# Kernel optimization log

Measured on AMD Instinct MI355X. Metric: run time of the kernel, lower is better.

Reference implementation:

```python
import jax, jax.numpy as jnp
import numpy as np

D_MODEL = 1024
NHEAD = 16
EPS = 1e-5


def pos_embed(x, pos):
    # Faithful, vectorized form of the sparse rotation matrix in the source.
    # Source builds rot[..., i, i+1] = sin(pos*i*omega) for even i and
    # rot[..., i, i-1] = cos(pos*i*omega) for odd i, then contracts the feature
    # dim of x against the rotation (intended einsum 'btf,btfd->btd').
    # Resulting column j: even j <- x[..., j+1]*cos(pos*(j+1)*omega),
    #                     odd  j <- x[..., j-1]*sin(pos*(j-1)*omega).
    d = x.shape[-1]
    omega = jnp.pi / d
    i_even = jnp.arange(0, d, 2, dtype=x.dtype)   # even rows -> odd output cols (sin)
    i_odd = jnp.arange(1, d, 2, dtype=x.dtype)    # odd rows  -> even output cols (cos)
    p = pos[..., None]  # (L,B,1)
    sin_part = jnp.sin(p * i_even * omega) * x[..., 0::2]  # -> odd columns
    cos_part = jnp.cos(p * i_odd * omega) * x[..., 1::2]   # -> even columns
    # interleave: even col = cos_part, odd col = sin_part
    return jnp.stack([cos_part, sin_part], axis=-1).reshape(x.shape)


def layer_norm_eps(x, w, b):
    # Source uses torch.var default (unbiased, ddof=1)
    mean = jnp.mean(x, axis=-1, keepdims=True)
    var = jnp.var(x, axis=-1, keepdims=True, ddof=1)
    return w * (x - mean) / jnp.sqrt(var + EPS) + b


def mha(q, k, v, w_qkv, b_qkv, w_o, b_o, nhead):
    L, B, E = q.shape
    S = k.shape[0]
    hd = E // nhead
    wq, wk, wv = jnp.split(w_qkv, 3, axis=0)
    bq, bk, bv = jnp.split(b_qkv, 3, axis=0)
    qp = (q @ wq.T + bq).reshape(L, B, nhead, hd).transpose(1, 2, 0, 3)  # (B,h,L,hd)
    kp = (k @ wk.T + bk).reshape(S, B, nhead, hd).transpose(1, 2, 0, 3)
    vp = (v @ wv.T + bv).reshape(S, B, nhead, hd).transpose(1, 2, 0, 3)
    scale = jnp.asarray(1.0 / np.sqrt(hd), q.dtype)
    scores = jnp.einsum('bhld,bhsd->bhls', qp, kp) * scale
    attn = jax.nn.softmax(scores, axis=-1)
    out = jnp.einsum('bhls,bhsd->bhld', attn, vp)
    out = out.transpose(2, 0, 1, 3).reshape(L, B, E) @ w_o.T + b_o
    ws = attn.mean(axis=1)  # average over heads, torch default
    return out, ws


def setup_inputs() -> dict:
    key = jax.random.key(0)
    ks = jax.random.split(key, 16)
    T, S, B, E, FF = 1024, 1024, 4, D_MODEL, 4096
    sd = 0.02
    return {
        'tgt': jax.random.normal(ks[0], (T, B, E), jnp.float32),
        'memory': jax.random.normal(ks[1], (S, B, E), jnp.float32),
        'pos': jax.random.uniform(ks[2], (S, B), jnp.float32) * S,
        'query_pos': jax.random.uniform(ks[3], (T, B), jnp.float32) * T,
        'w_qkv_self': jax.random.normal(ks[4], (3 * E, E), jnp.float32) * sd,
        'b_qkv_self': jnp.zeros((3 * E,), jnp.float32),
        'w_o_self': jax.random.normal(ks[5], (E, E), jnp.float32) * sd,
        'b_o_self': jnp.zeros((E,), jnp.float32),
        'w_qkv_cross': jax.random.normal(ks[6], (3 * E, E), jnp.float32) * sd,
        'b_qkv_cross': jnp.zeros((3 * E,), jnp.float32),
        'w_o_cross': jax.random.normal(ks[7], (E, E), jnp.float32) * sd,
        'b_o_cross': jnp.zeros((E,), jnp.float32),
        'w1': jax.random.normal(ks[8], (FF, E), jnp.float32) * sd,
        'b1': jnp.zeros((FF,), jnp.float32),
        'w2': jax.random.normal(ks[9], (E, FF), jnp.float32) * sd,
        'b2': jnp.zeros((E,), jnp.float32),
        'g1': jnp.ones((E,), jnp.float32),
        'beta1': jnp.zeros((E,), jnp.float32),
        'g2': jnp.ones((E,), jnp.float32),
        'beta2': jnp.zeros((E,), jnp.float32),
    }


def reference(tgt, memory, pos, query_pos,
              w_qkv_self, b_qkv_self, w_o_self, b_o_self,
              w_qkv_cross, b_qkv_cross, w_o_cross, b_o_cross,
              w1, b1, w2, b2, g1, beta1, g2, beta2):
    # normalize_before=False, residual=True, dropout inactive (eval)
    qk = pos_embed(tgt, query_pos)
    tgt2, _ = mha(qk, qk, tgt, w_qkv_self, b_qkv_self, w_o_self, b_o_self, NHEAD)
    tgt = tgt + tgt2
    tgt = layer_norm_eps(tgt, g1, beta1)
    tgt2, ws = mha(pos_embed(tgt, query_pos), pos_embed(memory, pos), memory,
                   w_qkv_cross, b_qkv_cross, w_o_cross, b_o_cross, NHEAD)
    tgt = tgt + tgt2
    tgt = layer_norm_eps(tgt, g2, beta2)
    tgt2 = jax.nn.relu(tgt @ w1.T + b1) @ w2.T + b2
    tgt = tgt + tgt2
    return tgt, ws
```

## Files before the change

### kernel.cpp

```cpp
#include <hip/hip_runtime.h>

typedef unsigned short u16;
typedef __attribute__((ext_vector_type(8))) short short8;
typedef __attribute__((ext_vector_type(8))) unsigned short u16x8;
typedef __attribute__((ext_vector_type(4))) float f32x4;

#define GLOAD16(SRC, DST) __builtin_amdgcn_global_load_lds( \
    (const __attribute__((address_space(1))) void*)(SRC),   \
    (__attribute__((address_space(3))) void*)(DST), 16, 0, 0)

#define SWZ(BKv, r) ((BKv) == 32 ? (((r) >> 1) & 3) : ((r) & 7))

#define QSCALE 0.18033688011112042f

__device__ __forceinline__ u16 f2bf(float f) {
  union { float f; unsigned u; } v; v.f = f;
  unsigned r = v.u + 0x7fffu + ((v.u >> 16) & 1u);
  return (u16)(r >> 16);
}
__device__ __forceinline__ float bf2f(u16 h) {
  union { unsigned u; float f; } v; v.u = ((unsigned)h) << 16;
  return v.f;
}

__global__ __launch_bounds__(256) void wcvt_kernel(const float* __restrict__ s0,
                                                   const float* __restrict__ s1,
                                                   const float* __restrict__ s2,
                                                   const float* __restrict__ s3,
                                                   const float* __restrict__ s4,
                                                   const float* __restrict__ s5,
                                                   u16* __restrict__ dst) {
  long i = ((long)blockIdx.x * 256 + threadIdx.x) * 4;
  const float* src; long off;
  if (i < 3145728)        { src = s0; off = 0; }
  else if (i < 4194304)   { src = s1; off = 3145728; }
  else if (i < 7340032)   { src = s2; off = 4194304; }
  else if (i < 8388608)   { src = s3; off = 7340032; }
  else if (i < 12582912)  { src = s4; off = 8388608; }
  else                    { src = s5; off = 12582912; }
  float4 v = *(const float4*)(src + (i - off));
  ushort4 o; o.x = f2bf(v.x); o.y = f2bf(v.y); o.z = f2bf(v.z); o.w = f2bf(v.w);
  *(ushort4*)(dst + i) = o;
}

__global__ __launch_bounds__(256) void pos_embed_kernel(const float* __restrict__ x,
                                                        const float* __restrict__ pos,
                                                        u16* __restrict__ out,
                                                        u16* __restrict__ out2,
                                                        u16* __restrict__ raw) {
  int m = blockIdx.x;
  int tid = threadIdx.x;
  float p = pos[m];
  long base = ((long)m << 10);
  int j = tid * 4;
  float4 xv = *(const float4*)(x + base + j);
  const float inv = 1.0f / 2048.0f;
  float r0 = p * (float)(j + 0) * inv;
  float r1 = p * (float)(j + 1) * inv;
  float r2 = p * (float)(j + 2) * inv;
  float r3 = p * (float)(j + 3) * inv;
  float s1 = __builtin_amdgcn_sinf(r0 - floorf(r0));
  float c0 = __builtin_amdgcn_cosf(r1 - floorf(r1));
  float s3 = __builtin_amdgcn_sinf(r2 - floorf(r2));
  float c2 = __builtin_amdgcn_cosf(r3 - floorf(r3));
  ushort4 o;
  o.x = f2bf(c0 * xv.y);
  o.y = f2bf(s1 * xv.x);
  o.z = f2bf(c2 * xv.w);
  o.w = f2bf(s3 * xv.z);
  *(ushort4*)(out + base + j) = o;
  if (out2) *(ushort4*)(out2 + base + j) = o;
  if (raw) {
    ushort4 rw; rw.x = f2bf(xv.x); rw.y = f2bf(xv.y); rw.z = f2bf(xv.z); rw.w = f2bf(xv.w);
    *(ushort4*)(raw + base + j) = rw;
  }
}

__global__ __launch_bounds__(256) void split_qkv_kernel(const u16* __restrict__ P,
                                                        u16* __restrict__ Qb,
                                                        u16* __restrict__ Kb,
                                                        u16* __restrict__ Vtb) {
  long e = ((long)blockIdx.x * 256 + threadIdx.x) * 8;
  int m = (int)(e / 3072);
  int n = (int)(e % 3072);
  int t = m >> 2, b = m & 3;
  int sec = n >> 10, nn = n & 1023;
  int h = nn >> 6, d = nn & 63;
  long bh = b * 16 + h;
  u16x8 v = *(const u16x8*)(P + e);
  if (sec == 0) {
    *(u16x8*)(Qb + (bh << 16) + ((long)t << 6) + d) = v;
  } else if (sec == 1) {
    *(u16x8*)(Kb + (bh << 16) + ((long)t << 6) + d) = v;
  } else {
    u16* dst = Vtb + (bh << 16) + ((long)d << 10) + t;
#pragma unroll
    for (int q = 0; q < 8; q++) dst[(long)q << 10] = v[q];
  }
}

__global__ __launch_bounds__(256) void fattn_kernel(const u16* __restrict__ Q,
                                                    const u16* __restrict__ K,
                                                    const u16* __restrict__ Vt,
                                                    u16* __restrict__ AO,
                                                    float2* __restrict__ Ml) {
  __shared__ u16 lK[2][4096];
  __shared__ u16 lV[2][4096];
  __shared__ u16 lP[4][1024];
  const int tid = threadIdx.x, lane = tid & 63, wid = tid >> 6;
  const int nb = gridDim.x * gridDim.y;
  const int orig = blockIdx.y * gridDim.x + blockIdx.x;
  const int swz = (orig & 7) * (nb >> 3) + (orig >> 3);
  const int qt = swz & 15;
  const int bh = swz >> 4;
  const int b = bh >> 4, h = bh & 15;
  const u16* Qp = Q + ((long)bh << 16);
  const u16* Kp = K + ((long)bh << 16);
  const u16* Vp = Vt + ((long)bh << 16);
  const int q0 = qt << 6;
  const int cr = lane >> 4;

  short8 af0, af1;
  {
    const u16* qs = Qp + (long)(q0 + wid * 16 + (lane & 15)) * 64 + cr * 8;
    af0 = *(const short8*)qs;
    af1 = *(const short8*)(qs + 32);
  }

  float m[4] = {-1e30f, -1e30f, -1e30f, -1e30f};
  float l[4] = {0.f, 0.f, 0.f, 0.f};
  f32x4 acco[4] = {};

  auto stage = [&](int bufi, int kv) {
    int s0 = kv << 6;
#pragma unroll
    for (int it = 0; it < 2; it++) {
      int c = it * 256 + tid;
      int row = c >> 3, ch = c & 7;
      int sch = (ch ^ (row & 7)) * 8;
      GLOAD16(Kp + (long)(s0 + row) * 64 + sch, &lK[bufi][c * 8]);
      GLOAD16(Vp + (long)row * 1024 + s0 + sch, &lV[bufi][c * 8]);
    }
  };

  stage(0, 0);
  __syncthreads();
  int buf = 0;
  for (int kv = 0; kv < 16; kv++) {
    if (kv < 15) stage(buf ^ 1, kv + 1);
    f32x4 accs[4];
    __builtin_amdgcn_s_setprio(1);
#pragma unroll
    for (int j = 0; j < 4; j++) {
      int sr = j * 16 + (lane & 15);
      const short8 kf0 = *(const short8*)&lK[buf][sr * 64 + ((cr ^ (sr & 7)) * 8)];
      const short8 kf1 = *(const short8*)&lK[buf][sr * 64 + (((4 + cr) ^ (sr & 7)) * 8)];
      f32x4 zz = {};
      zz = __builtin_amdgcn_mfma_f32_16x16x32_bf16(af0, kf0, zz, 0, 0, 0);
      accs[j] = __builtin_amdgcn_mfma_f32_16x16x32_bf16(af1, kf1, zz, 0, 0, 0);
    }
    __builtin_amdgcn_s_setprio(0);
    float tm[4];
#pragma unroll
    for (int r = 0; r < 4; r++)
      tm[r] = fmaxf(fmaxf(accs[0][r], accs[1][r]), fmaxf(accs[2][r], accs[3][r]));
#pragma unroll
    for (int o = 1; o < 16; o <<= 1)
#pragma unroll
      for (int r = 0; r < 4; r++) tm[r] = fmaxf(tm[r], __shfl_xor(tm[r], o));
    float growth = fmaxf(fmaxf(tm[0] - m[0], tm[1] - m[1]),
                         fmaxf(tm[2] - m[2], tm[3] - m[3]));
    if (!__all(growth <= 8.0f)) {
#pragma unroll
      for (int r = 0; r < 4; r++) {
        float mn = fmaxf(m[r], tm[r]);
        float f = __builtin_amdgcn_exp2f(m[r] - mn);
        m[r] = mn; l[r] *= f;
        acco[0][r] *= f; acco[1][r] *= f; acco[2][r] *= f; acco[3][r] *= f;
      }
    }
    float rs[4] = {0.f, 0.f, 0.f, 0.f};
#pragma unroll
    for (int j = 0; j < 4; j++)
#pragma unroll
      for (int r = 0; r < 4; r++) {
        float p = __builtin_amdgcn_exp2f(accs[j][r] - m[r]);
        accs[j][r] = p;
        rs[r] += p;
      }
#pragma unroll
    for (int o = 1; o < 16; o <<= 1)
#pragma unroll
      for (int r = 0; r < 4; r++) rs[r] += __shfl_xor(rs[r], o);
#pragma unroll
    for (int r = 0; r < 4; r++) l[r] += rs[r];
    u16* pw = lP[wid];
#pragma unroll
    for (int jp = 0; jp < 2; jp++)
#pragma unroll
      for (int r = 0; r < 4; r++) {
        int qr = (lane >> 4) * 4 + r;
        unsigned pk;
        asm("v_cvt_pk_bf16_f32 %0, %1, %2"
            : "=v"(pk) : "v"(accs[2 * jp][r]), "v"(accs[2 * jp + 1][r]));
        int sA = (2 * jp) * 16 + (lane & 15);
        int sB = sA + 16;
        pw[qr * 64 + (((sA >> 3) ^ (qr & 7)) * 8) + (sA & 7)] = (u16)pk;
        pw[qr * 64 + (((sB >> 3) ^ (qr & 7)) * 8) + (sB & 7)] = (u16)(pk >> 16);
      }
    {
      int ql = lane & 15;
      const u16* pr = &lP[wid][ql * 64];
      short8 pa0 = *(const short8*)&pr[(cr ^ (ql & 7)) * 8];
      short8 pa1 = *(const short8*)&pr[((4 + cr) ^ (ql & 7)) * 8];
      __builtin_amdgcn_s_setprio(1);
#pragma unroll
      for (int j = 0; j < 4; j++) {
        int dr = j * 16 + (lane & 15);
        const short8 vf0 = *(const short8*)&lV[buf][dr * 64 + ((cr ^ (dr & 7)) * 8)];
        const short8 vf1 = *(const short8*)&lV[buf][dr * 64 + (((4 + cr) ^ (dr & 7)) * 8)];
        acco[j] = __builtin_amdgcn_mfma_f32_16x16x32_bf16(pa0, vf0, acco[j], 0, 0, 0);
        acco[j] = __builtin_amdgcn_mfma_f32_16x16x32_bf16(pa1, vf1, acco[j], 0, 0, 0);
      }
      __builtin_amdgcn_s_setprio(0);
    }
    __syncthreads();
    buf ^= 1;
  }
  float invl[4];
#pragma unroll
  for (int r = 0; r < 4; r++) invl[r] = 1.0f / l[r];
#pragma unroll
  for (int j = 0; j < 4; j++)
#pragma unroll
    for (int r = 0; r < 4; r++) {
      int t = q0 + wid * 16 + (lane >> 4) * 4 + r;
      int e = (b << 10) + (h << 6) + j * 16 + (lane & 15);
      AO[(long)t * 4096 + e] = f2bf(acco[j][r] * invl[r]);
    }
  if (Ml && (lane & 15) == 0) {
#pragma unroll
    for (int r = 0; r < 4; r++) {
      int t = q0 + wid * 16 + (lane >> 4) * 4 + r;
      Ml[((long)bh << 10) + t] = make_float2(m[r], invl[r]);
    }
  }
}

__global__ __launch_bounds__(256) void wsrec_kernel(const u16* __restrict__ Q,
                                                    const u16* __restrict__ K,
                                                    const float2* __restrict__ Ml,
                                                    float* __restrict__ ws) {
  __shared__ u16 lK[2][4096];
  const int tid = threadIdx.x, lane = tid & 63, wid = tid >> 6;
  const int nb = gridDim.x * gridDim.y;
  const int orig = blockIdx.y * gridDim.x + blockIdx.x;
  const int swz = (orig & 7) * (nb >> 3) + (orig >> 3);
  const int st = swz & 15, lt = swz >> 4;
  const int b = blockIdx.z;
  const int s0 = st << 6, l0 = lt << 6;
  const int cr = lane >> 4;

  auto stage = [&](int bufi, int h) {
    const u16* Kp = K + (((long)(b * 16 + h)) << 16);
#pragma unroll
    for (int it = 0; it < 2; it++) {
      int c = it * 256 + tid;
      int row = c >> 3, ch = c & 7;
      GLOAD16(Kp + (long)(s0 + row) * 64 + ((ch ^ (row & 7)) * 8), &lK[bufi][c * 8]);
    }
  };

  f32x4 wacc[4] = {};
  stage(0, 0);
  __syncthreads();
  int buf = 0;
  for (int h = 0; h < 16; h++) {
    if (h < 15) stage(buf ^ 1, h + 1);
    const int bh = b * 16 + h;
    short8 af0, af1;
    {
      const u16* qs = Q + ((long)bh << 16) + (long)(l0 + wid * 16 + (lane & 15)) * 64 + cr * 8;
      af0 = *(const short8*)qs;
      af1 = *(const short8*)(qs + 32);
    }
    f32x4 accs[4];
    __builtin_amdgcn_s_setprio(1);
#pragma unroll
    for (int j = 0; j < 4; j++) {
      int sr = j * 16 + (lane & 15);
      const short8 kf0 = *(const short8*)&lK[buf][sr * 64 + ((cr ^ (sr & 7)) * 8)];
      const short8 kf1 = *(const short8*)&lK[buf][sr * 64 + (((4 + cr) ^ (sr & 7)) * 8)];
      f32x4 zz = {};
      zz = __builtin_amdgcn_mfma_f32_16x16x32_bf16(af0, kf0, zz, 0, 0, 0);
      accs[j] = __builtin_amdgcn_mfma_f32_16x16x32_bf16(af1, kf1, zz, 0, 0, 0);
    }
    __builtin_amdgcn_s_setprio(0);
    float mm[4], il[4];
#pragma unroll
    for (int r = 0; r < 4; r++) {
      float2 v = Ml[((long)bh << 10) + l0 + wid * 16 + (lane >> 4) * 4 + r];
      mm[r] = v.x; il[r] = v.y * 0.0625f;
    }
#pragma unroll
    for (int j = 0; j < 4; j++)
#pragma unroll
      for (int r = 0; r < 4; r++)
        wacc[j][r] += __builtin_amdgcn_exp2f(accs[j][r] - mm[r]) * il[r];
    __syncthreads();
    buf ^= 1;
  }
#pragma unroll
  for (int j = 0; j < 4; j++)
#pragma unroll
    for (int r = 0; r < 4; r++) {
      int li = l0 + wid * 16 + (lane >> 4) * 4 + r;
      int si = s0 + j * 16 + (lane & 15);
      ws[((long)b << 20) + (long)li * 1024 + si] = wacc[j][r];
    }
}

__global__ __launch_bounds__(256) void ln_kernel(const float* __restrict__ X,
                                                 const float* __restrict__ D1,
                                                 const float* __restrict__ D2,
                                                 const float* __restrict__ bo,
                                                 const float* __restrict__ g,
                                                 const float* __restrict__ be,
                                                 float* __restrict__ out,
                                                 u16* __restrict__ bfout) {
  int mrow = blockIdx.x;
  int tid = threadIdx.x, lane = tid & 63, wid = tid >> 6;
  long base = ((long)mrow << 10);
  float4 a = *(const float4*)(X + base + tid * 4);
  float4 b = *(const float4*)(D1 + base + tid * 4);
  float x0 = a.x + b.x, x1 = a.y + b.y, x2 = a.z + b.z, x3 = a.w + b.w;
  if (D2) {
    float4 c = *(const float4*)(D2 + base + tid * 4);
    x0 += c.x; x1 += c.y; x2 += c.z; x3 += c.w;
  }
  if (bo) {
    float4 c = *(const float4*)(bo + tid * 4);
    x0 += c.x; x1 += c.y; x2 += c.z; x3 += c.w;
  }
  float s = x0 + x1 + x2 + x3;
#pragma unroll
  for (int o = 32; o; o >>= 1) s += __shfl_xor(s, o);
  __shared__ float red[4];
  if (lane == 0) red[wid] = s;
  __syncthreads();
  float mean = (red[0] + red[1] + red[2] + red[3]) * (1.0f / 1024.0f);
  float d0 = x0 - mean, d1 = x1 - mean, d2 = x2 - mean, d3 = x3 - mean;
  float ss = d0 * d0 + d1 * d1 + d2 * d2 + d3 * d3;
#pragma unroll
  for (int o = 32; o; o >>= 1) ss += __shfl_xor(ss, o);
  __syncthreads();
  if (lane == 0) red[wid] = ss;
  __syncthreads();
  float var = (red[0] + red[1] + red[2] + red[3]) * (1.0f / 1023.0f);
  float sc = 1.0f / sqrtf(var + 1e-5f);
  float4 gv = *(const float4*)(g + tid * 4);
  float4 bv = *(const float4*)(be + tid * 4);
  float y0 = gv.x * d0 * sc + bv.x;
  float y1 = gv.y * d1 * sc + bv.y;
  float y2 = gv.z * d2 * sc + bv.z;
  float y3 = gv.w * d3 * sc + bv.w;
  float4 o4; o4.x = y0; o4.y = y1; o4.z = y2; o4.w = y3;
  *(float4*)(out + base + tid * 4) = o4;
  if (bfout) {
    ushort4 hh; hh.x = f2bf(y0); hh.y = f2bf(y1); hh.z = f2bf(y2); hh.w = f2bf(y3);
    *(ushort4*)(bfout + base + tid * 4) = hh;
  }
}

__global__ __launch_bounds__(256) void add3_kernel(const float* __restrict__ X,
                                                   const float* __restrict__ P0,
                                                   const float* __restrict__ P1,
                                                   const float* __restrict__ b,
                                                   float* __restrict__ out) {
  long i = ((long)blockIdx.x * 256 + threadIdx.x) * 4;
  int col = (int)(i & 1023);
  float4 x = *(const float4*)(X + i);
  float4 p = *(const float4*)(P0 + i);
  float4 q = *(const float4*)(P1 + i);
  float4 bb = *(const float4*)(b + col);
  float4 o;
  o.x = x.x + p.x + q.x + bb.x;
  o.y = x.y + p.y + q.y + bb.y;
  o.z = x.z + p.z + q.z + bb.z;
  o.w = x.w + p.w + q.w + bb.w;
  *(float4*)(out + i) = o;
}

template <int BM, int BN, int BK, int WR, int WC, int NT, int DB>
__global__ __launch_bounds__(NT)
void gemm_bt_kernel(const u16* __restrict__ A, const u16* __restrict__ B,
                    void* __restrict__ C, const float* __restrict__ bias,
                    int lda, int ldb, int ldc, int K,
                    long sAz, long sBz, long sCz, long sbz,
                    float alpha, int flags) {
  constexpr int WTM = BM / WR, WTN = BN / WC;
  constexpr int FM = WTM / 16, FN = WTN / 16;
  constexpr int NC = BK / 8;
  __shared__ u16 lA[DB][BM * BK];
  __shared__ u16 lB[DB][BN * BK];
  const int tid = threadIdx.x, lane = tid & 63, wid = tid >> 6;
  const int wr = wid / WC, wc = wid % WC;
  const int z = blockIdx.z;

  const int nwg = gridDim.x * gridDim.y;
  const int orig = blockIdx.y * gridDim.x + blockIdx.x;
  const int qq = nwg >> 3, rr = nwg & 7;
  const int xcd = orig & 7, idx = orig >> 3;
  const int swz = (xcd < rr ? xcd * (qq + 1) : rr * (qq + 1) + (xcd - rr) * qq) + idx;
  const int bxs = swz % gridDim.x;
  const int bys = swz / gridDim.x;

  const u16* Ab = A + z * sAz + (long)bys * BM * lda;
  const u16* Bb = B + z * sBz + (long)bxs * BN * ldb;

  f32x4 acc[FM][FN] = {};

  auto stage = [&](int bufi, int k0) {
#pragma unroll
    for (int c0 = 0; c0 < BM * NC; c0 += NT) {
      int c = c0 + tid;
      if ((BM * NC) % NT == 0 || c < BM * NC) {
        int row = c / NC, ch = c % NC;
        int sch = ch ^ SWZ(BK, row);
        GLOAD16(Ab + (long)row * lda + k0 + sch * 8, &lA[bufi][c * 8]);
      }
    }
#pragma unroll
    for (int c0 = 0; c0 < BN * NC; c0 += NT) {
      int c = c0 + tid;
      if ((BN * NC) % NT == 0 || c < BN * NC) {
        int row = c / NC, ch = c % NC;
        int sch = ch ^ SWZ(BK, row);
        GLOAD16(Bb + (long)row * ldb + k0 + sch * 8, &lB[bufi][c * 8]);
      }
    }
  };

  auto compute = [&](int bufi) {
#pragma unroll
    for (int kk = 0; kk < BK / 32; kk++) {
      short8 afv[FM], bfv[FN];
#pragma unroll
      for (int i = 0; i < FM; i++) {
        int row = wr * WTM + i * 16 + (lane & 15);
        int ch = kk * 4 + (lane >> 4);
        afv[i] = *(const short8*)&lA[bufi][row * BK + ((ch ^ SWZ(BK, row)) * 8)];
      }
#pragma unroll
      for (int j = 0; j < FN; j++) {
        int row = wc * WTN + j * 16 + (lane & 15);
        int ch = kk * 4 + (lane >> 4);
        bfv[j] = *(const short8*)&lB[bufi][row * BK + ((ch ^ SWZ(BK, row)) * 8)];
      }
#pragma unroll
      for (int i = 0; i < FM; i++)
#pragma unroll
        for (int j = 0; j < FN; j++)
          acc[i][j] = __builtin_amdgcn_mfma_f32_16x16x32_bf16(afv[i], bfv[j], acc[i][j], 0, 0, 0);
    }
  };

  const int nk = K / BK;
  if (DB == 2) {
    stage(0, 0);
    __syncthreads();
    int cur = 0;
    for (int t = 0; t < nk; t++) {
      if (t + 1 < nk) stage(cur ^ 1, (t + 1) * BK);
      compute(cur);
      __syncthreads();
      cur ^= 1;
    }
  } else {
    for (int t = 0; t < nk; t++) {
      stage(0, t * BK);
      __syncthreads();
      compute(0);
      __syncthreads();
    }
  }

  const long rbase = (long)bys * BM + wr * WTM;
  const int cbase = bxs * BN + wc * WTN;
  const float* bz = bias ? (bias + z * sbz) : nullptr;
#pragma unroll
  for (int i = 0; i < FM; i++)
#pragma unroll
    for (int j = 0; j < FN; j++)
#pragma unroll
      for (int r = 0; r < 4; r++) {
        long row = rbase + i * 16 + ((lane >> 4) * 4 + r);
        int col = cbase + j * 16 + (lane & 15);
        float v = acc[i][j][r];
        if (!(flags & 8)) v *= alpha;
        if (flags & 1) v += bz[col];
        if ((flags & 8) && z == 0) v *= alpha;
        if (flags & 2) v = fmaxf(v, 0.0f);
        long off = (long)z * sCz + row * (long)ldc + col;
        if (flags & 4) ((float*)C)[off] = v;
        else ((u16*)C)[off] = f2bf(v);
      }
}

extern "C" void kernel_launch(void* const* d_in, const int* in_sizes, int n_in,
                              void* d_out, int out_size, void* d_ws, size_t ws_size,
                              hipStream_t stream) {
  const float* tgt  = (const float*)d_in[0];
  const float* mem  = (const float*)d_in[1];
  const float* pos  = (const float*)d_in[2];
  const float* qpos = (const float*)d_in[3];
  const float* wqkvS = (const float*)d_in[4];
  const float* bqkvS = (const float*)d_in[5];
  const float* woS   = (const float*)d_in[6];
  const float* boS   = (const float*)d_in[7];
  const float* wqkvC = (const float*)d_in[8];
  const float* bqkvC = (const float*)d_in[9];
  const float* woC   = (const float*)d_in[10];
  const float* boC   = (const float*)d_in[11];
  const float* w1  = (const float*)d_in[12];
  const float* b1  = (const float*)d_in[13];
  const float* w2  = (const float*)d_in[14];
  const float* b2  = (const float*)d_in[15];
  const float* g1  = (const float*)d_in[16];
  const float* be1 = (const float*)d_in[17];
  const float* g2  = (const float*)d_in[18];
  const float* be2 = (const float*)d_in[19];

  const size_t MB = 1024ull * 1024ull;
  float* out0 = (float*)d_out;
  float* wsout = out0 + 4194304;

  char* W = (char*)d_ws;
  u16* wb = (u16*)W;
  u16* wqkvS_b = wb;
  u16* woS_b   = wb + 3145728;
  u16* wqkvC_b = wb + 4194304;
  u16* woC_b   = wb + 7340032;
  u16* w1_b    = wb + 8388608;
  u16* w2_b    = wb + 12582912;
  float* Xf   = (float*)(W + 32 * MB);
  float* OPar = (float*)(W + 48 * MB);
  u16* Pq  = (u16*)(W + 48 * MB);
  u16* bf1 = (u16*)(W + 80 * MB);
  u16* bf2 = (u16*)(W + 88 * MB);
  u16* bf3 = (u16*)(W + 96 * MB);
  float2* Ml = (float2*)(W + 96 * MB);
  u16* Qb  = (u16*)(W + 104 * MB);
  u16* Kb  = (u16*)(W + 112 * MB);
  u16* Vtb = (u16*)(W + 120 * MB);
  u16* AOb = (u16*)(W + 128 * MB);
  u16* F1  = (u16*)(W + 104 * MB);

  wcvt_kernel<<<16384, 256, 0, stream>>>(wqkvS, woS, wqkvC, woC, w1, w2, wb);

  pos_embed_kernel<<<4096, 256, 0, stream>>>(tgt, qpos, bf1, bf2, bf3);
  gemm_bt_kernel<128, 128, 32, 2, 4, 512, 2><<<dim3(8, 32, 3), 512, 0, stream>>>(
      bf1, wqkvS_b, Pq, bqkvS, 1024, 1024, 3072, 1024,
      4194304, 1048576, 1024, 1024, QSCALE, 1 | 8);
  split_qkv_kernel<<<6144, 256, 0, stream>>>(Pq, Qb, Kb, Vtb);
  fattn_kernel<<<dim3(16, 64), 256, 0, stream>>>(Qb, Kb, Vtb, AOb, nullptr);
  gemm_bt_kernel<128, 128, 32, 2, 4, 512, 2><<<dim3(8, 32, 2), 512, 0, stream>>>(
      AOb, woS_b, OPar, nullptr, 1024, 1024, 1024, 512,
      512, 512, 4194304, 0, 1.0f, 4);
  ln_kernel<<<4096, 256, 0, stream>>>(tgt, OPar, OPar + 4194304, boS, g1, be1, Xf, nullptr);

  pos_embed_kernel<<<4096, 256, 0, stream>>>(Xf, qpos, bf1, nullptr, nullptr);
  pos_embed_kernel<<<4096, 256, 0, stream>>>(mem, pos, bf2, nullptr, bf3);
  gemm_bt_kernel<128, 128, 32, 2, 4, 512, 2><<<dim3(8, 32, 3), 512, 0, stream>>>(
      bf1, wqkvC_b, Pq, bqkvC, 1024, 1024, 3072, 1024,
      4194304, 1048576, 1024, 1024, QSCALE, 1 | 8);
  split_qkv_kernel<<<6144, 256, 0, stream>>>(Pq, Qb, Kb, Vtb);
  fattn_kernel<<<dim3(16, 64), 256, 0, stream>>>(Qb, Kb, Vtb, AOb, Ml);
  wsrec_kernel<<<dim3(16, 16, 4), 256, 0, stream>>>(Qb, Kb, Ml, wsout);
  gemm_bt_kernel<128, 128, 32, 2, 4, 512, 2><<<dim3(8, 32, 2), 512, 0, stream>>>(
      AOb, woC_b, OPar, nullptr, 1024, 1024, 1024, 512,
      512, 512, 4194304, 0, 1.0f, 4);
  ln_kernel<<<4096, 256, 0, stream>>>(Xf, OPar, OPar + 4194304, boC, g2, be2, Xf, bf1);

  gemm_bt_kernel<128, 128, 32, 2, 4, 512, 2><<<dim3(32, 32, 1), 512, 0, stream>>>(
      bf1, w1_b, F1, b1, 1024, 1024, 4096, 1024, 0, 0, 0, 0, 1.0f, 1 | 2);
  gemm_bt_kernel<128, 128, 32, 2, 4, 512, 2><<<dim3(8, 32, 2), 512, 0, stream>>>(
      F1, w2_b, OPar, nullptr, 4096, 4096, 1024, 2048,
      2048, 2048, 4194304, 0, 1.0f, 4);
  add3_kernel<<<4096, 256, 0, stream>>>(Xf, OPar, OPar + 4194304, b2, out0);
}
```

Measured before the change: 473.8 us.

## Transpose QK^T MFMA operands in flash attention and raise GEMM K-tile

The flash-attention kernel swaps the A and B operands of the score MFMA, so each lane now holds one query row's scores across four keys. The row max and row sum then need only two cross-lane shuffles instead of a 16-lane butterfly over four rows, and P is written to LDS as packed 64-bit stores instead of scattered 16-bit stores. Per-row rescale factors and the final 1/l are broadcast with __shfl to match the transposed output layout. Separately, four of the GEMM launches (QKV projections, FFN1, FFN2) move from a K-tile of 32 to 64, which halves the K-loop iterations but uses more LDS per block and may lower occupancy.

```diff
diff --git a/kernel.cpp b/kernel.cpp
--- a/kernel.cpp
+++ b/kernel.cpp
@@ -127,8 +127,7 @@
     af1 = *(const short8*)(qs + 32);
   }
 
-  float m[4] = {-1e30f, -1e30f, -1e30f, -1e30f};
-  float l[4] = {0.f, 0.f, 0.f, 0.f};
+  float m = -1e30f, l = 0.f;
   f32x4 acco[4] = {};
 
   auto stage = [&](int bufi, int kv) {
@@ -156,58 +155,56 @@
       const short8 kf0 = *(const short8*)&lK[buf][sr * 64 + ((cr ^ (sr & 7)) * 8)];
       const short8 kf1 = *(const short8*)&lK[buf][sr * 64 + (((4 + cr) ^ (sr & 7)) * 8)];
       f32x4 zz = {};
-      zz = __builtin_amdgcn_mfma_f32_16x16x32_bf16(af0, kf0, zz, 0, 0, 0);
-      accs[j] = __builtin_amdgcn_mfma_f32_16x16x32_bf16(af1, kf1, zz, 0, 0, 0);
+      zz = __builtin_amdgcn_mfma_f32_16x16x32_bf16(kf0, af0, zz, 0, 0, 0);
+      accs[j] = __builtin_amdgcn_mfma_f32_16x16x32_bf16(kf1, af1, zz, 0, 0, 0);
     }
     __builtin_amdgcn_s_setprio(0);
-    float tm[4];
-#pragma unroll
-    for (int r = 0; r < 4; r++)
-      tm[r] = fmaxf(fmaxf(accs[0][r], accs[1][r]), fmaxf(accs[2][r], accs[3][r]));
-#pragma unroll
-    for (int o = 1; o < 16; o <<= 1)
-#pragma unroll
-      for (int r = 0; r < 4; r++) tm[r] = fmaxf(tm[r], __shfl_xor(tm[r], o));
-    float growth = fmaxf(fmaxf(tm[0] - m[0], tm[1] - m[1]),
-                         fmaxf(tm[2] - m[2], tm[3] - m[3]));
-    if (!__all(growth <= 8.0f)) {
+    float tm = fmaxf(fmaxf(fmaxf(accs[0][0], accs[0][1]), fmaxf(accs[0][2], accs[0][3])),
+                     fmaxf(fmaxf(accs[1][0], accs[1][1]), fmaxf(accs[1][2], accs[1][3])));
+    float tm2 = fmaxf(fmaxf(fmaxf(accs[2][0], accs[2][1]), fmaxf(accs[2][2], accs[2][3])),
+                      fmaxf(fmaxf(accs[3][0], accs[3][1]), fmaxf(accs[3][2], accs[3][3])));
+    tm = fmaxf(tm, tm2);
+    tm = fmaxf(tm, __shfl_xor(tm, 16));
+    tm = fmaxf(tm, __shfl_xor(tm, 32));
+    if (!__all(tm - m <= 8.0f)) {
+      float mn = fmaxf(m, tm);
+      float f = __builtin_amdgcn_exp2f(m - mn);
+      m = mn; l *= f;
 #pragma unroll
       for (int r = 0; r < 4; r++) {
-        float mn = fmaxf(m[r], tm[r]);
-        float f = __builtin_amdgcn_exp2f(m[r] - mn);
-        m[r] = mn; l[r] *= f;
-        acco[0][r] *= f; acco[1][r] *= f; acco[2][r] *= f; acco[3][r] *= f;
-      }
-    }
-    float rs[4] = {0.f, 0.f, 0.f, 0.f};
+        float fr = __shfl(f, cr * 4 + r);
+        acco[0][r] *= fr; acco[1][r] *= fr; acco[2][r] *= fr; acco[3][r] *= fr;
+      }
+    }
+    float rs = 0.f;
 #pragma unroll
     for (int j = 0; j < 4; j++)
 #pragma unroll
       for (int r = 0; r < 4; r++) {
-        float p = __builtin_amdgcn_exp2f(accs[j][r] - m[r]);
+        float p = __builtin_amdgcn_exp2f(accs[j][r] - m);
         accs[j][r] = p;
-        rs[r] += p;
-      }
-#pragma unroll
-    for (int o = 1; o < 16; o <<= 1)
-#pragma unroll
-      for (int r = 0; r < 4; r++) rs[r] += __shfl_xor(rs[r], o);
-#pragma unroll
-    for (int r = 0; r < 4; r++) l[r] += rs[r];
-    u16* pw = lP[wid];
-#pragma unroll
-    for (int jp = 0; jp < 2; jp++)
-#pragma unroll
-      for (int r = 0; r < 4; r++) {
-        int qr = (lane >> 4) * 4 + r;
-        unsigned pk;
+        rs += p;
+      }
+    rs += __shfl_xor(rs, 16);
+    rs += __shfl_xor(rs, 32);
+    l += rs;
+    {
+      u16* pw = lP[wid];
+      int q = lane & 15;
+      int rowoff = q * 64;
+      int qs7 = q & 7;
+#pragma unroll
+      for (int j = 0; j < 4; j++) {
+        uint2 pk;
         asm("v_cvt_pk_bf16_f32 %0, %1, %2"
-            : "=v"(pk) : "v"(accs[2 * jp][r]), "v"(accs[2 * jp + 1][r]));
-        int sA = (2 * jp) * 16 + (lane & 15);
-        int sB = sA + 16;
-        pw[qr * 64 + (((sA >> 3) ^ (qr & 7)) * 8) + (sA & 7)] = (u16)pk;
-        pw[qr * 64 + (((sB >> 3) ^ (qr & 7)) * 8) + (sB & 7)] = (u16)(pk >> 16);
-      }
+            : "=v"(pk.x) : "v"(accs[j][0]), "v"(accs[j][1]));
+        asm("v_cvt_pk_bf16_f32 %0, %1, %2"
+            : "=v"(pk.y) : "v"(accs[j][2]), "v"(accs[j][3]));
+        int chunk = 2 * j + (cr >> 1);
+        int idx = rowoff + ((chunk ^ qs7) * 8) + 4 * (cr & 1);
+        *(uint2*)(pw + idx) = pk;
+      }
+    }
     {
       int ql = lane & 15;
       const u16* pr = &lP[wid][ql * 64];
@@ -227,23 +224,21 @@
     __syncthreads();
     buf ^= 1;
   }
-  float invl[4];
-#pragma unroll
-  for (int r = 0; r < 4; r++) invl[r] = 1.0f / l[r];
+  float invl = 1.0f / l;
+  float ilr[4];
+#pragma unroll
+  for (int r = 0; r < 4; r++) ilr[r] = __shfl(invl, cr * 4 + r);
 #pragma unroll
   for (int j = 0; j < 4; j++)
 #pragma unroll
     for (int r = 0; r < 4; r++) {
-      int t = q0 + wid * 16 + (lane >> 4) * 4 + r;
+      int t = q0 + wid * 16 + cr * 4 + r;
       int e = (b << 10) + (h << 6) + j * 16 + (lane & 15);
-      AO[(long)t * 4096 + e] = f2bf(acco[j][r] * invl[r]);
-    }
-  if (Ml && (lane & 15) == 0) {
-#pragma unroll
-    for (int r = 0; r < 4; r++) {
-      int t = q0 + wid * 16 + (lane >> 4) * 4 + r;
-      Ml[((long)bh << 10) + t] = make_float2(m[r], invl[r]);
-    }
+      AO[(long)t * 4096 + e] = f2bf(acco[j][r] * ilr[r]);
+    }
+  if (Ml && lane < 16) {
+    int t = q0 + wid * 16 + lane;
+    Ml[((long)bh << 10) + t] = make_float2(m, invl);
   }
 }
 
@@ -559,7 +554,7 @@
   wcvt_kernel<<<16384, 256, 0, stream>>>(wqkvS, woS, wqkvC, woC, w1, w2, wb);
 
   pos_embed_kernel<<<4096, 256, 0, stream>>>(tgt, qpos, bf1, bf2, bf3);
-  gemm_bt_kernel<128, 128, 32, 2, 4, 512, 2><<<dim3(8, 32, 3), 512, 0, stream>>>(
+  gemm_bt_kernel<128, 128, 64, 2, 4, 512, 2><<<dim3(8, 32, 3), 512, 0, stream>>>(
       bf1, wqkvS_b, Pq, bqkvS, 1024, 1024, 3072, 1024,
       4194304, 1048576, 1024, 1024, QSCALE, 1 | 8);
   split_qkv_kernel<<<6144, 256, 0, stream>>>(Pq, Qb, Kb, Vtb);
@@ -571,7 +566,7 @@
 
   pos_embed_kernel<<<4096, 256, 0, stream>>>(Xf, qpos, bf1, nullptr, nullptr);
   pos_embed_kernel<<<4096, 256, 0, stream>>>(mem, pos, bf2, nullptr, bf3);
-  gemm_bt_kernel<128, 128, 32, 2, 4, 512, 2><<<dim3(8, 32, 3), 512, 0, stream>>>(
+  gemm_bt_kernel<128, 128, 64, 2, 4, 512, 2><<<dim3(8, 32, 3), 512, 0, stream>>>(
       bf1, wqkvC_b, Pq, bqkvC, 1024, 1024, 3072, 1024,
       4194304, 1048576, 1024, 1024, QSCALE, 1 | 8);
   split_qkv_kernel<<<6144, 256, 0, stream>>>(Pq, Qb, Kb, Vtb);
@@ -582,9 +577,9 @@
       512, 512, 4194304, 0, 1.0f, 4);
   ln_kernel<<<4096, 256, 0, stream>>>(Xf, OPar, OPar + 4194304, boC, g2, be2, Xf, bf1);
 
-  gemm_bt_kernel<128, 128, 32, 2, 4, 512, 2><<<dim3(32, 32, 1), 512, 0, stream>>>(
+  gemm_bt_kernel<128, 128, 64, 2, 4, 512, 2><<<dim3(32, 32, 1), 512, 0, stream>>>(
       bf1, w1_b, F1, b1, 1024, 1024, 4096, 1024, 0, 0, 0, 0, 1.0f, 1 | 2);
-  gemm_bt_kernel<128, 128, 32, 2, 4, 512, 2><<<dim3(8, 32, 2), 512, 0, stream>>>(
+  gemm_bt_kernel<128, 128, 64, 2, 4, 512, 2><<<dim3(8, 32, 2), 512, 0, stream>>>(
       F1, w2_b, OPar, nullptr, 4096, 4096, 1024, 2048,
       2048, 2048, 4194304, 0, 1.0f, 4);
   add3_kernel<<<4096, 256, 0, stream>>>(Xf, OPar, OPar + 4194304, b2, out0);
```

Result: faster. 448.6 us (-5.3%).
